# Performance work log

Measured on AMD Instinct MI355X. Metric: run time of the kernel, lower is better.

The kernel has to match this reference:

```python
import jax, jax.numpy as jnp
import numpy as np

N_POINTS = 500_000
N_CENTERS = 1000
DIM = 128


def setup_inputs() -> dict:
    key = jax.random.key(0)
    k1, k2, k3 = jax.random.split(key, 3)
    x = jax.random.normal(k1, (N_POINTS, DIM), dtype=jnp.float32)
    y = jax.random.randint(k2, (N_POINTS,), 0, N_CENTERS, dtype=jnp.int64)
    centers = jax.random.normal(k3, (N_CENTERS, DIM), dtype=jnp.float32)
    counter = jnp.ones((1,), dtype=jnp.float32)
    return {"x": x, "y": y, "centers": centers, "counter": counter}


def reference(x, y, centers, counter):
    """Faithful vectorized version of RunningCenters.forward (training mode).

    Original: per-class mean via Python loop over unique classes, then a
    cumulative-moving-average update of the running centers for classes
    present in the batch. Here: one scatter-add pass (segment_sum of values
    and of counts) gives per-class means in O(N); a masked CMA update
    replaces the indexed scatter write.
    Returns the updated centers buffer [C, D].
    """
    C, D = centers.shape
    # per-class sum and count in a single streaming pass over x
    sums = jax.ops.segment_sum(x, y, num_segments=C)                      # [C, D]
    counts = jax.ops.segment_sum(jnp.ones((x.shape[0],), x.dtype), y,
                                 num_segments=C)                           # [C]
    present = counts > 0                                                   # which classes appear in batch
    mu = sums / jnp.maximum(counts, 1.0)[:, None]                          # safe mean (0 for absent classes)
    # cumulative moving average: centers[c] <- (mu[c] + centers[c]*counter) / (counter + 1)
    cma = (mu + centers * counter) / (counter + 1.0)                       # broadcast counter [1]
    new_centers = jnp.where(present[:, None], cma, centers)
    return new_centers
```

## Files before the change

### kernel.cpp

```cpp
#include <hip/hip_runtime.h>


constexpr int C = 1000;
constexpr int D = 128;
constexpr int CAP = 1024;
constexpr int SB = 256;
constexpr int ST = 512;
constexpr int TILE = 2048;
constexpr int CST = 512;

typedef float f4 __attribute__((ext_vector_type(4)));


__global__ __launch_bounds__(1024) void zero_kernel(
    unsigned int* __restrict__ cur) {
  cur[threadIdx.x] = 0u;
}

__global__ __launch_bounds__(ST) void scatter_kernel(
    const int* __restrict__ y, unsigned int* __restrict__ cur,
    int* __restrict__ sorted, int N, int chunk) {
  const int b = blockIdx.x;
  const int beg = b * chunk;
  const int e = min(beg + chunk, N);
  for (int i = beg + threadIdx.x; i < e; i += ST) {
    const int c = y[i];
    const unsigned int p = atomicAdd(&cur[c], 1u);
    if (p < (unsigned int)CAP) sorted[c * CAP + p] = i;
  }
}

__global__ __launch_bounds__(CST) void class_sum_kernel(
    const float* __restrict__ x, const int* __restrict__ sorted,
    const unsigned int* __restrict__ cur,
    const float* __restrict__ centers, const float* __restrict__ counter,
    float* __restrict__ out) {
  const int c = blockIdx.x;
  const int begin = c * CAP;
  const int n = min((int)cur[c], CAP);
  const int wave = threadIdx.x >> 6;
  const int lane = threadIdx.x & 63;
  const int half = lane >> 5;
  const int d4 = lane & 31;

  __shared__ int idx[TILE];
  __shared__ f4 red[8][64];
  f4 acc = (f4)(0.f);

  for (int t0 = 0; t0 < n; t0 += TILE) {
    const int nt = min(TILE, n - t0);
    __syncthreads();
    for (int t = threadIdx.x; t < nt; t += CST) idx[t] = sorted[begin + t0 + t];
    __syncthreads();
    const int npair = nt >> 1;
    int q = wave;
    for (; q + 56 < npair; q += 64) {
#pragma unroll
      for (int u = 0; u < 8; ++u) {
        const int p = (q + 8 * u) * 2 + half;
        f4 v = __builtin_nontemporal_load(
            (const f4*)(x + (size_t)idx[p] * D) + d4);
        acc += v;
      }
    }
    for (; q < npair; q += 8) {
      const int p = q * 2 + half;
      f4 v = __builtin_nontemporal_load(
          (const f4*)(x + (size_t)idx[p] * D) + d4);
      acc += v;
    }
    if ((nt & 1) && wave == 0 && half == 0) {
      f4 v = __builtin_nontemporal_load(
          (const f4*)(x + (size_t)idx[nt - 1] * D) + d4);
      acc += v;
    }
  }

  red[wave][lane] = acc;
  __syncthreads();
  if (threadIdx.x < 32) {
    const int l = threadIdx.x;
    f4 s = (f4)(0.f);
#pragma unroll
    for (int w = 0; w < 8; ++w) s += red[w][l] + red[w][l + 32];
    const f4 cen = ((const f4*)centers)[c * 32 + l];
    f4 o;
    if (n > 0) {
      const float k = counter[0];
      const float inv = 1.f / (float)n;
      const float ik = 1.f / (k + 1.f);
      o = (s * inv + cen * k) * ik;
    } else {
      o = cen;
    }
    ((f4*)out)[c * 32 + l] = o;
  }
}

extern "C" void kernel_launch(void* const* d_in, const int* in_sizes, int n_in,
                              void* d_out, int out_size, void* d_ws, size_t ws_size,
                              hipStream_t stream) {
  const float* x       = (const float*)d_in[0];
  const int* y         = (const int*)d_in[1];
  const float* centers = (const float*)d_in[2];
  const float* counter = (const float*)d_in[3];
  float* out = (float*)d_out;
  const int N = in_sizes[1];

  unsigned int* cur = (unsigned int*)d_ws;
  int* sorted       = (int*)((char*)d_ws + 4096);

  const int chunk = (N + SB - 1) / SB;

  zero_kernel<<<dim3(1), dim3(1024), 0, stream>>>(cur);
  scatter_kernel<<<dim3(SB), dim3(ST), 0, stream>>>(y, cur, sorted, N, chunk);
  class_sum_kernel<<<dim3(C), dim3(CST), 0, stream>>>(x, sorted, cur,
                                                      centers, counter, out);
}
```

Before: 429.4 us.

## Replace counting-sort gather with LDS atomic per-partition class sums plus reduction

Drops the bucket-by-class scatter and the per-class gather of rows. Each block now streams a contiguous slice of points and accumulates a 32-column slice of every class sum in shared memory with float atomics, plus a class histogram. A second kernel adds up the 64 partition partials per class and applies the moving-average update. This gives coalesced, sequential reads of x instead of random row gathers and removes the per-class capacity cap. In exchange it relies on LDS float atomics under possible same-class contention, uses 128 KB of shared memory per block, writes about 32 MB of partials, and reads y four times.

```diff
diff --git a/kernel.cpp b/kernel.cpp
--- a/kernel.cpp
+++ b/kernel.cpp
@@ -3,98 +3,100 @@
 
 constexpr int C = 1000;
 constexpr int D = 128;
-constexpr int CAP = 1024;
-constexpr int SB = 256;
-constexpr int ST = 512;
-constexpr int TILE = 2048;
-constexpr int CST = 512;
+constexpr int PARTS = 64;
+constexpr int CHUNKS = 4;
+constexpr int DC = 32;
+constexpr int AT = 1024;
+constexpr int NW = AT / 64;
+constexpr int RT = 128;
 
 typedef float f4 __attribute__((ext_vector_type(4)));
 
 
-__global__ __launch_bounds__(1024) void zero_kernel(
-    unsigned int* __restrict__ cur) {
-  cur[threadIdx.x] = 0u;
+__global__ __launch_bounds__(AT) void accum_kernel(
+    const float* __restrict__ x, const int* __restrict__ y,
+    float* __restrict__ partial, unsigned int* __restrict__ histp, int N) {
+  const int part = blockIdx.x >> 2;
+  const int chunk = blockIdx.x & 3;
+  const int d0 = chunk * DC;
+
+  __shared__ float sums[C * DC];
+  __shared__ unsigned int hist[C];
+  for (int t = threadIdx.x; t < C * DC; t += AT) sums[t] = 0.f;
+  if (chunk == 0)
+    for (int t = threadIdx.x; t < C; t += AT) hist[t] = 0u;
+  __syncthreads();
+
+  const int per = (N + PARTS - 1) / PARTS;
+  const int beg = part * per;
+  const int end = min(beg + per, N);
+  const int wave = threadIdx.x >> 6;
+  const int lane = threadIdx.x & 63;
+  const int half = lane >> 5;
+  const int dl = lane & 31;
+
+  const int stride = NW * 2;
+  int i = beg + wave * 2 + half;
+  for (; i + 7 * stride < end; i += 8 * stride) {
+#pragma unroll
+    for (int u = 0; u < 8; ++u) {
+      const int ii = i + u * stride;
+      const int c = y[ii];
+      const float v = x[(size_t)ii * D + d0 + dl];
+      atomicAdd(&sums[c * DC + dl], v);
+      if (chunk == 0 && dl == 0) atomicAdd(&hist[c], 1u);
+    }
+  }
+  for (; i < end; i += stride) {
+    const int c = y[i];
+    const float v = x[(size_t)i * D + d0 + dl];
+    atomicAdd(&sums[c * DC + dl], v);
+    if (chunk == 0 && dl == 0) atomicAdd(&hist[c], 1u);
+  }
+
+  __syncthreads();
+  f4* dst = (f4*)(partial + (size_t)blockIdx.x * (C * DC));
+  const f4* src = (const f4*)sums;
+  for (int t = threadIdx.x; t < C * DC / 4; t += AT) dst[t] = src[t];
+  if (chunk == 0)
+    for (int t = threadIdx.x; t < C; t += AT)
+      histp[t * PARTS + part] = hist[t];
 }
 
-__global__ __launch_bounds__(ST) void scatter_kernel(
-    const int* __restrict__ y, unsigned int* __restrict__ cur,
-    int* __restrict__ sorted, int N, int chunk) {
-  const int b = blockIdx.x;
-  const int beg = b * chunk;
-  const int e = min(beg + chunk, N);
-  for (int i = beg + threadIdx.x; i < e; i += ST) {
-    const int c = y[i];
-    const unsigned int p = atomicAdd(&cur[c], 1u);
-    if (p < (unsigned int)CAP) sorted[c * CAP + p] = i;
-  }
-}
-
-__global__ __launch_bounds__(CST) void class_sum_kernel(
-    const float* __restrict__ x, const int* __restrict__ sorted,
-    const unsigned int* __restrict__ cur,
+__global__ __launch_bounds__(RT) void reduce_kernel(
+    const float* __restrict__ partial, const unsigned int* __restrict__ histp,
     const float* __restrict__ centers, const float* __restrict__ counter,
     float* __restrict__ out) {
   const int c = blockIdx.x;
-  const int begin = c * CAP;
-  const int n = min((int)cur[c], CAP);
-  const int wave = threadIdx.x >> 6;
-  const int lane = threadIdx.x & 63;
-  const int half = lane >> 5;
-  const int d4 = lane & 31;
+  const int d = threadIdx.x;
+  const int chunk = d >> 5;
+  const int dd = d & 31;
 
-  __shared__ int idx[TILE];
-  __shared__ f4 red[8][64];
-  f4 acc = (f4)(0.f);
+  __shared__ unsigned int nsh;
+  if (d < 64) {
+    unsigned int v = histp[c * PARTS + d];
+#pragma unroll
+    for (int off = 32; off; off >>= 1) v += __shfl_down(v, off, 64);
+    if (d == 0) nsh = v;
+  }
+  __syncthreads();
+  const int n = (int)nsh;
 
-  for (int t0 = 0; t0 < n; t0 += TILE) {
-    const int nt = min(TILE, n - t0);
-    __syncthreads();
-    for (int t = threadIdx.x; t < nt; t += CST) idx[t] = sorted[begin + t0 + t];
-    __syncthreads();
-    const int npair = nt >> 1;
-    int q = wave;
-    for (; q + 56 < npair; q += 64) {
-#pragma unroll
-      for (int u = 0; u < 8; ++u) {
-        const int p = (q + 8 * u) * 2 + half;
-        f4 v = __builtin_nontemporal_load(
-            (const f4*)(x + (size_t)idx[p] * D) + d4);
-        acc += v;
-      }
-    }
-    for (; q < npair; q += 8) {
-      const int p = q * 2 + half;
-      f4 v = __builtin_nontemporal_load(
-          (const f4*)(x + (size_t)idx[p] * D) + d4);
-      acc += v;
-    }
-    if ((nt & 1) && wave == 0 && half == 0) {
-      f4 v = __builtin_nontemporal_load(
-          (const f4*)(x + (size_t)idx[nt - 1] * D) + d4);
-      acc += v;
-    }
+  const size_t base = (size_t)chunk * (C * DC) + c * DC + dd;
+  float s = 0.f;
+#pragma unroll 8
+  for (int p = 0; p < PARTS; ++p)
+    s += partial[base + (size_t)p * (CHUNKS * C * DC)];
+
+  const float cen = centers[c * D + d];
+  float o;
+  if (n > 0) {
+    const float k = counter[0];
+    o = (s / (float)n + cen * k) / (k + 1.f);
+  } else {
+    o = cen;
   }
-
-  red[wave][lane] = acc;
-  __syncthreads();
-  if (threadIdx.x < 32) {
-    const int l = threadIdx.x;
-    f4 s = (f4)(0.f);
-#pragma unroll
-    for (int w = 0; w < 8; ++w) s += red[w][l] + red[w][l + 32];
-    const f4 cen = ((const f4*)centers)[c * 32 + l];
-    f4 o;
-    if (n > 0) {
-      const float k = counter[0];
-      const float inv = 1.f / (float)n;
-      const float ik = 1.f / (k + 1.f);
-      o = (s * inv + cen * k) * ik;
-    } else {
-      o = cen;
-    }
-    ((f4*)out)[c * 32 + l] = o;
-  }
+  out[c * D + d] = o;
 }
 
 extern "C" void kernel_launch(void* const* d_in, const int* in_sizes, int n_in,
@@ -107,13 +109,11 @@
   float* out = (float*)d_out;
   const int N = in_sizes[1];
 
-  unsigned int* cur = (unsigned int*)d_ws;
-  int* sorted       = (int*)((char*)d_ws + 4096);
+  float* partial      = (float*)d_ws;
+  unsigned int* histp = (unsigned int*)((char*)d_ws + (33u << 20));
 
-  const int chunk = (N + SB - 1) / SB;
-
-  zero_kernel<<<dim3(1), dim3(1024), 0, stream>>>(cur);
-  scatter_kernel<<<dim3(SB), dim3(ST), 0, stream>>>(y, cur, sorted, N, chunk);
-  class_sum_kernel<<<dim3(C), dim3(CST), 0, stream>>>(x, sorted, cur,
-                                                      centers, counter, out);
+  accum_kernel<<<dim3(PARTS * CHUNKS), dim3(AT), 0, stream>>>(x, y, partial,
+                                                              histp, N);
+  reduce_kernel<<<dim3(C), dim3(RT), 0, stream>>>(partial, histp, centers,
+                                                  counter, out);
 }
```

After: 612.3 us. 42.6% more time.
